# Kernel optimization log

Hardware: AMD Instinct MI355X
Metric: run time of the kernel (lower is better)

Reference implementation:

```python
import jax, jax.numpy as jnp
import numpy as np

K = 16                 # k nearest neighbors
POS_LO, POS_HI = 0, 3  # position_slice
INF = jnp.float32(1e30)


def setup_inputs() -> dict:
    key = jax.random.key(0)
    k1, k2, k3 = jax.random.split(key, 3)
    B, N, F = 16, 2048, 128
    nodes = jax.random.normal(k1, (B, N, F), dtype=jnp.float32)
    T = jax.random.randint(k2, (B,), 0, 1024)
    taus = jax.random.randint(k3, (B,), 0, 1024)
    return {"nodes": nodes, "T": T, "taus": taus, "B": B}


def reference(nodes, T, taus, B):
    # Faithful, vectorized version of the per-batch causal KNN edge builder.
    # Original: for each batch b, sinks = pos[b, T[b]:T[b]+taus[b]],
    # sources = pos[b, :T[b]+taus[b]]; knn(source, sink, k) returns
    # (sink_local_idx, source_idx); keep edges where sink_local > source;
    # assemble COO adjacency (b, sink_local, source) with weight 1.
    # Here we return the equivalent DENSE [B, N, N] adjacency.
    pos = nodes[:, :, POS_LO:POS_HI]              # [B, N, d]
    N = pos.shape[1]
    i_idx = jnp.arange(N)                         # local sink index grid
    # global index of sink i in batch b is T[b] + i
    sink_gidx = jnp.clip(T[:, None] + i_idx[None, :], 0, N - 1)   # [B, N]
    sink_pos = jnp.take_along_axis(pos, sink_gidx[..., None], axis=1)  # [B, N, d]
    sink_valid = i_idx[None, :] < taus[:, None]                    # [B, N]
    src_valid = i_idx[None, :] < (T + taus)[:, None]               # [B, N]
    # squared distances sink->source: [B, N_sink, N_src]
    d2 = jnp.sum((sink_pos[:, :, None, :] - pos[:, None, :, :]) ** 2, axis=-1)
    d2 = jnp.where(src_valid[:, None, :], d2, INF)
    neg_vals, nbr = jax.lax.top_k(-d2, K)          # k smallest distances, [B, N, K]
    nbr_valid = neg_vals > -INF                    # source actually existed
    causal = i_idx[None, :, None] > nbr            # edge[0] > edge[1] mask (local sink idx)
    valid = sink_valid[:, :, None] & nbr_valid & causal
    adj = jnp.zeros((B, N, N), dtype=jnp.float32)
    b_idx = jnp.arange(B)[:, None, None]
    adj = adj.at[b_idx, i_idx[None, :, None], nbr].add(
        jnp.where(valid, jnp.float32(1.0), jnp.float32(0.0)))
    return adj
```

## Files before the change

### kernel.cpp

```cpp
#include <hip/hip_runtime.h>

#define NN 2048
#define FF 128
#define KK 16
#define INF_KEY 0xFFFFFFFFFFFFFFFFull

typedef float f32x4 __attribute__((ext_vector_type(4)));

__device__ __forceinline__ unsigned wave_min_u32(unsigned x) {
    int v = (int)x, t;
    t = __builtin_amdgcn_update_dpp(v, v, 0x111, 0xf, 0xf, false);
    v = ((unsigned)t < (unsigned)v) ? t : v;
    t = __builtin_amdgcn_update_dpp(v, v, 0x112, 0xf, 0xf, false);
    v = ((unsigned)t < (unsigned)v) ? t : v;
    t = __builtin_amdgcn_update_dpp(v, v, 0x114, 0xf, 0xf, false);
    v = ((unsigned)t < (unsigned)v) ? t : v;
    t = __builtin_amdgcn_update_dpp(v, v, 0x118, 0xf, 0xf, false);
    v = ((unsigned)t < (unsigned)v) ? t : v;
    t = __builtin_amdgcn_update_dpp(v, v, 0x142, 0xf, 0xf, false);
    v = ((unsigned)t < (unsigned)v) ? t : v;
    t = __builtin_amdgcn_update_dpp(v, v, 0x143, 0xf, 0xf, false);
    v = ((unsigned)t < (unsigned)v) ? t : v;
    return (unsigned)__builtin_amdgcn_readlane(v, 63);
}

__global__ __launch_bounds__(256) void pack_xyz(
    const float* __restrict__ nodes, f32x4* __restrict__ out, int total)
{
    const int t = blockIdx.x * 256 + threadIdx.x;
    if (t < total) {
        const float* p = nodes + (size_t)t * FF;
        out[t] = (f32x4){p[0], p[1], p[2], 0.f};
    }
}

template<bool PACKED>
__device__ __forceinline__ f32x4 load_xyz(const float* __restrict__ base, int idx) {
    if constexpr (PACKED) {
        return ((const f32x4*)base)[idx];
    } else {
        const float* p = base + (size_t)idx * FF;
        return (f32x4){p[0], p[1], p[2], 0.f};
    }
}

template<bool PACKED>
__global__ __launch_bounds__(256, 8) void knn_adj_fused(
    const float* __restrict__ xyz,
    const int*   __restrict__ T_arr,
    const int*   __restrict__ tau_arr,
    float*       __restrict__ adj)
{
    const int b    = blockIdx.x;
    const int i0   = blockIdx.y << 2;
    const int tid  = threadIdx.x;
    const int wave = tid >> 6;
    const int lane = tid & 63;

    const int tau = tau_arr[b];
    float* block_out = adj + ((size_t)b * NN + i0) * NN;

    if (i0 >= tau) {
        const f32x4 z = (f32x4){0.f, 0.f, 0.f, 0.f};
        f32x4* out4 = (f32x4*)block_out;
        #pragma unroll
        for (int t = 0; t < 8; ++t)
            __builtin_nontemporal_store(z, &out4[tid + (t << 8)]);
        return;
    }

    const int i = i0 + wave;
    f32x4* out4 = (f32x4*)(block_out + (size_t)wave * NN);

    if (i >= tau) {
        const f32x4 z = (f32x4){0.f, 0.f, 0.f, 0.f};
        #pragma unroll
        for (int t = 0; t < 8; ++t)
            __builtin_nontemporal_store(z, &out4[(t << 6) + lane]);
        return;
    }

    const int T = T_arr[b];
    const int M = T + tau;
    const float* base = PACKED ? xyz + (size_t)b * NN * 4
                               : xyz + (size_t)b * NN * FF;
    __shared__ unsigned swords[4][64];

    const int g = T + i;
    const f32x4 sp = load_xyz<PACKED>(base, g);
    const float sxv = sp.x, syv = sp.y, szv = sp.z;

    unsigned long long q0 = INF_KEY, q1 = INF_KEY, q2 = INF_KEY, q3 = INF_KEY;
    const int S = (M + 63) >> 6;
    #pragma unroll 4
    for (int s = 0; s < S; ++s) {
        const int j = lane + (s << 6);
        if (j < M) {
            const f32x4 v = load_xyz<PACKED>(base, j);
            float dx = __fsub_rn(sxv, v.x);
            float dy = __fsub_rn(syv, v.y);
            float dz = __fsub_rn(szv, v.z);
            float d2 = __fadd_rn(__fadd_rn(__fmul_rn(dx, dx), __fmul_rn(dy, dy)),
                                 __fmul_rn(dz, dz));
            unsigned long long key =
                ((unsigned long long)__float_as_uint(d2) << 32) | (unsigned)(j + 1);
            if (key < q3) {
                q3 = key;
                unsigned long long t;
                if (q3 < q2) { t = q2; q2 = q3; q3 = t; }
                if (q2 < q1) { t = q1; q1 = q2; q2 = t; }
                if (q1 < q0) { t = q0; q0 = q1; q1 = t; }
            }
        }
    }

    unsigned colmask = 0;
    unsigned long long lastpop = 0;
    for (int k = 0; k < KK; ++k) {
        const unsigned hd = (unsigned)(q0 >> 32);
        const unsigned m  = wave_min_u32(hd);
        if (m == 0xFFFFFFFFu) break;

        const unsigned long long mask = __ballot(hd == m);
        unsigned jwin;
        if (__popcll(mask) == 1) {
            const int w = __builtin_ctzll(mask);
            jwin = (unsigned)__builtin_amdgcn_readlane((int)(unsigned)q0, w);
        } else {
            unsigned jc = (hd == m) ? (unsigned)q0 : 0xFFFFFFFFu;
            jwin = wave_min_u32(jc);
        }
        const int j = (int)jwin - 1;

        if (j < i && (j >> 5) == lane)
            colmask |= 1u << (j & 31);

        if (hd == m && (unsigned)q0 == jwin) {
            lastpop = ((unsigned long long)m << 32) | jwin;
            q0 = q1; q1 = q2; q2 = q3; q3 = INF_KEY;
            if (q0 == INF_KEY) {
                unsigned long long best = INF_KEY;
                for (int s2 = 0; s2 < S; ++s2) {
                    const int jj = lane + (s2 << 6);
                    if (jj < M) {
                        const f32x4 v = load_xyz<PACKED>(base, jj);
                        float dx = __fsub_rn(sxv, v.x);
                        float dy = __fsub_rn(syv, v.y);
                        float dz = __fsub_rn(szv, v.z);
                        float d2 = __fadd_rn(
                            __fadd_rn(__fmul_rn(dx, dx), __fmul_rn(dy, dy)),
                            __fmul_rn(dz, dz));
                        unsigned long long kk =
                            ((unsigned long long)__float_as_uint(d2) << 32)
                            | (unsigned)(jj + 1);
                        if (kk > lastpop && kk < best) best = kk;
                    }
                }
                q0 = best;
            }
        }
    }

    swords[wave][lane] = colmask;
    #pragma unroll
    for (int k = 0; k < 8; ++k) {
        const unsigned w   = swords[wave][(k << 3) + (lane >> 3)];
        const unsigned nib = (w >> ((lane & 7) << 2)) & 0xFu;
        f32x4 v;
        v.x = (nib & 1u) ? 1.0f : 0.0f;
        v.y = (nib & 2u) ? 1.0f : 0.0f;
        v.z = (nib & 4u) ? 1.0f : 0.0f;
        v.w = (nib & 8u) ? 1.0f : 0.0f;
        __builtin_nontemporal_store(v, &out4[(k << 6) + lane]);
    }
}

extern "C" void kernel_launch(void* const* d_in, const int* in_sizes, int n_in,
                              void* d_out, int out_size, void* d_ws, size_t ws_size,
                              hipStream_t stream) {
    const float* nodes = (const float*)d_in[0];
    const int*   T     = (const int*)d_in[1];
    const int*   taus  = (const int*)d_in[2];
    float*       adj   = (float*)d_out;
    const int B = in_sizes[1];

    dim3 grid(B, NN / 4);
    const size_t need = (size_t)B * NN * sizeof(f32x4);

    if (d_ws != nullptr && ws_size >= need) {
        const int total = B * NN;
        pack_xyz<<<dim3((total + 255) / 256), dim3(256), 0, stream>>>(
            nodes, (f32x4*)d_ws, total);
        knn_adj_fused<true><<<grid, dim3(256), 0, stream>>>(
            (const float*)d_ws, T, taus, adj);
    } else {
        knn_adj_fused<false><<<grid, dim3(256), 0, stream>>>(
            nodes, T, taus, adj);
    }
}
```

Measured before the change: 286.9 us.

## Zero output with memset and scatter KNN edges from one lane

Replaces the kernel's per-row dense zero/one stores with a hipMemsetAsync of the full adjacency, followed by scattered single-float writes of the neighbor edges. The grid is also shrunk to cover only sink rows below 1024, which assumes taus never exceeds that bound. This removes the shared-memory bitmask expansion and the in-kernel zero writes, at the cost of a separate memset pass and uncoalesced scatter stores.

```diff
diff --git a/kernel.cpp b/kernel.cpp
--- a/kernel.cpp
+++ b/kernel.cpp
@@ -45,7 +45,7 @@
 }
 
 template<bool PACKED>
-__global__ __launch_bounds__(256, 8) void knn_adj_fused(
+__global__ __launch_bounds__(256, 8) void knn_scatter(
     const float* __restrict__ xyz,
     const int*   __restrict__ T_arr,
     const int*   __restrict__ tau_arr,
@@ -58,33 +58,16 @@
     const int lane = tid & 63;
 
     const int tau = tau_arr[b];
-    float* block_out = adj + ((size_t)b * NN + i0) * NN;
-
-    if (i0 >= tau) {
-        const f32x4 z = (f32x4){0.f, 0.f, 0.f, 0.f};
-        f32x4* out4 = (f32x4*)block_out;
-        #pragma unroll
-        for (int t = 0; t < 8; ++t)
-            __builtin_nontemporal_store(z, &out4[tid + (t << 8)]);
-        return;
-    }
+    if (i0 >= tau) return;
 
     const int i = i0 + wave;
-    f32x4* out4 = (f32x4*)(block_out + (size_t)wave * NN);
-
-    if (i >= tau) {
-        const f32x4 z = (f32x4){0.f, 0.f, 0.f, 0.f};
-        #pragma unroll
-        for (int t = 0; t < 8; ++t)
-            __builtin_nontemporal_store(z, &out4[(t << 6) + lane]);
-        return;
-    }
+    if (i >= tau) return;
 
     const int T = T_arr[b];
     const int M = T + tau;
     const float* base = PACKED ? xyz + (size_t)b * NN * 4
                                : xyz + (size_t)b * NN * FF;
-    __shared__ unsigned swords[4][64];
+    float* row = adj + ((size_t)b * NN + i) * NN;
 
     const int g = T + i;
     const f32x4 sp = load_xyz<PACKED>(base, g);
@@ -114,7 +97,6 @@
         }
     }
 
-    unsigned colmask = 0;
     unsigned long long lastpop = 0;
     for (int k = 0; k < KK; ++k) {
         const unsigned hd = (unsigned)(q0 >> 32);
@@ -132,8 +114,8 @@
         }
         const int j = (int)jwin - 1;
 
-        if (j < i && (j >> 5) == lane)
-            colmask |= 1u << (j & 31);
+        if (lane == 0 && j < i)
+            row[j] = 1.0f;
 
         if (hd == m && (unsigned)q0 == jwin) {
             lastpop = ((unsigned long long)m << 32) | jwin;
@@ -160,19 +142,6 @@
             }
         }
     }
-
-    swords[wave][lane] = colmask;
-    #pragma unroll
-    for (int k = 0; k < 8; ++k) {
-        const unsigned w   = swords[wave][(k << 3) + (lane >> 3)];
-        const unsigned nib = (w >> ((lane & 7) << 2)) & 0xFu;
-        f32x4 v;
-        v.x = (nib & 1u) ? 1.0f : 0.0f;
-        v.y = (nib & 2u) ? 1.0f : 0.0f;
-        v.z = (nib & 4u) ? 1.0f : 0.0f;
-        v.w = (nib & 8u) ? 1.0f : 0.0f;
-        __builtin_nontemporal_store(v, &out4[(k << 6) + lane]);
-    }
 }
 
 extern "C" void kernel_launch(void* const* d_in, const int* in_sizes, int n_in,
@@ -184,17 +153,19 @@
     float*       adj   = (float*)d_out;
     const int B = in_sizes[1];
 
-    dim3 grid(B, NN / 4);
+    const size_t out_bytes = (size_t)B * NN * NN * sizeof(float);
+    hipMemsetAsync(adj, 0, out_bytes, stream);
+
+    dim3 grid(B, 1024 / 4);
     const size_t need = (size_t)B * NN * sizeof(f32x4);
-
     if (d_ws != nullptr && ws_size >= need) {
         const int total = B * NN;
         pack_xyz<<<dim3((total + 255) / 256), dim3(256), 0, stream>>>(
             nodes, (f32x4*)d_ws, total);
-        knn_adj_fused<true><<<grid, dim3(256), 0, stream>>>(
+        knn_scatter<true><<<grid, dim3(256), 0, stream>>>(
             (const float*)d_ws, T, taus, adj);
     } else {
-        knn_adj_fused<false><<<grid, dim3(256), 0, stream>>>(
+        knn_scatter<false><<<grid, dim3(256), 0, stream>>>(
             nodes, T, taus, adj);
     }
 }
```

Result: slower. 312.4 us (+8.9%).
